# Kernel tuning notes

Hardware: AMD Instinct MI355X
Metric: run time of the kernel (lower is better)

Reference implementation:

```python
import jax, jax.numpy as jnp
import numpy as np

INPUT_DIM = 1024
OUTPUT_DIM = 1000
DEPTH = 10
LAMBDA_REG = 1e-3
N_INTERNAL = 2 ** DEPTH - 1
N_LEAF = 2 ** DEPTH
BATCH = 16384


def setup_inputs() -> dict:
    key = jax.random.key(0)
    k1, k2, k3 = jax.random.split(key, 3)
    X = jax.random.normal(k1, (BATCH, INPUT_DIM), dtype=jnp.float32)
    # torch nn.Linear weight layout: [out_features, in_features]; scaled to keep
    # sigmoid routing probs away from 0/1 saturation (log-reg term).
    W_internal = jax.random.normal(k2, (N_INTERNAL, INPUT_DIM + 1), dtype=jnp.float32) * 0.02
    W_leaf = jax.random.normal(k3, (OUTPUT_DIM, N_LEAF), dtype=jnp.float32) * 0.02
    return {"X": X, "W_internal": W_internal, "W_leaf": W_leaf}


def _tree_paths(X, W_internal):
    B = X.shape[0]
    Xb = jnp.concatenate([jnp.ones((B, 1), X.dtype), X], axis=1)  # [B, D+1]
    logits = jax.nn.sigmoid(Xb @ W_internal.T)                    # [B, N_int]
    routing = jnp.stack([logits, 1.0 - logits], axis=2)           # [B, N_int, 2]
    path = jnp.ones((B, 1), X.dtype)
    reg = jnp.float32(0.0)
    start = 0
    for layer in range(DEPTH):
        n = 2 ** layer
        lp = routing[:, start:start + n, :].reshape(B, 2 * n)     # next_paths [B, 2n]
        path = jnp.repeat(path, 2, axis=1) * lp                   # new path probs [B, 2n]
        # Faithful to source: parent_idx = node_idx // 2 indexes the UPDATED path probs.
        parent = jnp.repeat(path[:, :n], 2, axis=1)               # [B, 2n]
        num = jnp.sum(lp * parent, axis=0)                        # [2n]
        den = jnp.sum(parent, axis=0) + 1e-8                      # [2n]
        alpha = num / den
        factor = LAMBDA_REG * 2.0 ** (-layer)
        reg = reg + factor * jnp.sum(-0.5 * (jnp.log(alpha) + jnp.log(1.0 - alpha)))
        start += n
    return path, reg  # path: [B, 2^DEPTH]


def reference(X, W_internal, W_leaf):
    path_probs, reg = _tree_paths(X, W_internal)
    predictions = path_probs @ W_leaf.T   # [B, output_dim]
    return predictions, reg
```

## Files before the change

kernel.cpp:

```cpp
#include <hip/hip_runtime.h>
#include <hip/hip_bf16.h>

#define B_ROWS 16384
#define K_DIM  1024
#define N_INT  1023
#define N_OUT  1000

using s8vec = __attribute__((ext_vector_type(8))) short;
using f32x4 = __attribute__((ext_vector_type(4))) float;

static const size_t OFF_XB   = 0;
static const size_t OFF_W1   = OFF_XB   + 33554432;
static const size_t OFF_BIAS = OFF_W1   + 2097152;
static const size_t OFF_PROB = OFF_BIAS + 4096;
static const size_t OFF_PATH = OFF_PROB + 33554432;
static const size_t OFF_W2   = OFF_PATH + 33554432;
static const size_t OFF_SG   = OFF_W2   + 2097152;
static const size_t OFF_TKT  = OFF_SG   + 16384;

__device__ __forceinline__ float b2f(ushort u) {
  return __uint_as_float(((unsigned)u) << 16);
}
__device__ __forceinline__ float blo(unsigned u) { return __uint_as_float(u << 16); }
__device__ __forceinline__ float bhi(unsigned u) { return __uint_as_float(u & 0xffff0000u); }
__device__ __forceinline__ ushort f2b(float f) {
  unsigned u = __float_as_uint(f);
  u = u + 0x7FFFu + ((u >> 16) & 1u);
  return (ushort)(u >> 16);
}

__device__ __forceinline__ void load_lds16(const ushort* g, ushort* l) {
  __builtin_amdgcn_global_load_lds((const __attribute__((address_space(1))) void*)g,
                                   (__attribute__((address_space(3))) void*)l,
                                   16, 0, 0);
}

__global__ __launch_bounds__(256) void cvt_all(const float4* __restrict__ X,
                                               ushort4* __restrict__ O,
                                               const float* __restrict__ Wi,
                                               const float* __restrict__ Wl,
                                               ushort* __restrict__ W1,
                                               ushort* __restrict__ W2,
                                               float* __restrict__ bias,
                                               float* __restrict__ Sg,
                                               unsigned* __restrict__ ticket) {
  const int b = blockIdx.x;
  if (b < 16384) {
    const int i = b * 256 + threadIdx.x;
    const float4 v = X[i];
    ushort4 o;
    o.x = f2b(v.x); o.y = f2b(v.y); o.z = f2b(v.z); o.w = f2b(v.w);
    O[i] = o;
  } else if (b < 24576) {
    const int idx = (b - 16384) * 256 + threadIdx.x;
    if (idx < (1 << 20)) {
      const int n = idx >> 10, k = idx & 1023;
      const float v = (n < N_INT) ? Wi[n * 1025 + 1 + k] : 0.f;
      W1[idx] = f2b(v);
      if (k == 0) bias[n] = (n < N_INT) ? Wi[n * 1025] : 0.f;
    } else {
      const int j = idx - (1 << 20);
      const int n = j >> 10, k = j & 1023;
      const float v = (n < N_OUT) ? Wl[n * 1024 + k] : 0.f;
      W2[j] = f2b(v);
    }
  } else {
#pragma unroll
    for (int k = 0; k < 16; ++k) Sg[threadIdx.x + 256 * k] = 0.f;
    if (threadIdx.x == 0) *ticket = 0u;
  }
}

template <int MODE>
__global__ __launch_bounds__(256, 5) void gemm_bt(const ushort* __restrict__ A,
                                                  const ushort* __restrict__ Bm,
                                                  const float* __restrict__ bias,
                                                  void* __restrict__ outp) {
  __shared__ ushort As[2][4096];
  __shared__ ushort Bs[2][4096];
  const int tid = threadIdx.x;
  const int bm = blockIdx.x, bn = blockIdx.y;
  const int lane = tid & 63, wv = tid >> 6;
  const int wm = wv >> 1, wn = wv & 1;
  const int m16 = lane & 15, q = lane >> 4;
  const int qs = q ^ ((m16 >> 1) & 3);

  const int r0 = tid >> 2;
  const int qsw = (tid & 3) ^ ((r0 >> 1) & 3);
  const ushort* aG = A  + (size_t)(bm * 128 + r0) * 1024 + qsw * 8;
  const ushort* bG = Bm + (size_t)(bn * 128 + r0) * 1024 + qsw * 8;

  f32x4 acc[4][4] = {};

#define STAGE(buf, kk) do {                                   \
    load_lds16(aG + (kk), As[buf] + wv * 512);                \
    load_lds16(aG + 65536 + (kk), As[buf] + 2048 + wv * 512); \
    load_lds16(bG + (kk), Bs[buf] + wv * 512);                \
    load_lds16(bG + 65536 + (kk), Bs[buf] + 2048 + wv * 512); \
  } while (0)

#define COMPUTE(cur) do {                                                        \
    s8vec af[4], bfv[4];                                                         \
    _Pragma("unroll")                                                            \
    for (int i = 0; i < 4; ++i)                                                  \
      af[i] = *(const s8vec*)(As[cur] + (wm * 64 + i * 16 + m16) * 32 + qs * 8); \
    _Pragma("unroll")                                                            \
    for (int j = 0; j < 4; ++j)                                                  \
      bfv[j] = *(const s8vec*)(Bs[cur] + (wn * 64 + j * 16 + m16) * 32 + qs * 8);\
    _Pragma("unroll")                                                            \
    for (int i = 0; i < 4; ++i)                                                  \
      _Pragma("unroll")                                                          \
      for (int j = 0; j < 4; ++j)                                                \
        acc[i][j] = __builtin_amdgcn_mfma_f32_16x16x32_bf16(af[i], bfv[j],       \
                                                            acc[i][j], 0, 0, 0);\
  } while (0)

  STAGE(0, 0);
#pragma unroll 1
  for (int k0 = 0; k0 < 992; k0 += 32) {
    const int cur = (k0 >> 5) & 1;
    STAGE(cur ^ 1, k0 + 32);
    asm volatile("s_waitcnt vmcnt(4)\n\ts_barrier" ::: "memory");
    COMPUTE(cur);
    asm volatile("s_barrier" ::: "memory");
  }
  asm volatile("s_waitcnt vmcnt(0)\n\ts_barrier" ::: "memory");
  COMPUTE(1);
#undef STAGE
#undef COMPUTE

  if (MODE == 0) {
    ushort* P = (ushort*)outp;
#pragma unroll
    for (int i = 0; i < 4; ++i)
#pragma unroll
      for (int r = 0; r < 4; ++r) {
        const int gr = bm * 128 + wm * 64 + i * 16 + q * 4 + r;
#pragma unroll
        for (int j = 0; j < 4; ++j) {
          const int gc = bn * 128 + wn * 64 + j * 16 + m16;
          const float z = acc[i][j][r] + bias[gc];
          const float p = __builtin_amdgcn_rcpf(1.f + __expf(-z));
          if (gc < N_INT) P[(size_t)gr * 1024 + gc + 1] = f2b(p);
        }
      }
  } else {
    float* O = (float*)outp;
#pragma unroll
    for (int i = 0; i < 4; ++i)
#pragma unroll
      for (int r = 0; r < 4; ++r) {
        const int gr = bm * 128 + wm * 64 + i * 16 + q * 4 + r;
#pragma unroll
        for (int j = 0; j < 4; ++j) {
          const int gc = bn * 128 + wn * 64 + j * 16 + m16;
          if (gc < N_OUT) O[(size_t)gr * 1000 + gc] = acc[i][j][r];
        }
      }
  }
}

__global__ __launch_bounds__(256) void tree_kernel(const ushort* __restrict__ probs,
                                                   ushort* __restrict__ path,
                                                   float* __restrict__ Spart) {
  __shared__ float Ss[2048];
  for (int i = threadIdx.x; i < 2048; i += 256) Ss[i] = 0.f;
  __syncthreads();
  const int lane = threadIdx.x & 63;
  const int la = lane & 31;
  const int gw = blockIdx.x * 4 + (threadIdx.x >> 6);

  float a19[16] = {}, a29[16] = {};
  float a18[8]  = {}, a28[8]  = {};
  float a17[4]  = {}, a27[4]  = {};
  float a16[2]  = {}, a26[2]  = {};
  float t1[6] = {}, t2[6] = {};

#pragma unroll 1
  for (int rr = 0; rr < 4; ++rr) {
    const int r = gw * 4 + rr;
    const ushort* prow = probs + (size_t)r * 1024;

    const ushort p6 = prow[64 + lane];
    const uint   p7 = *(const uint*)(prow + 128 + 2 * lane);
    const uint2  p8 = *(const uint2*)(prow + 256 + 4 * lane);
    const uint4  p9 = *(const uint4*)(prow + 512 + 8 * lane);
    union { uint4 q[2]; ushort u[16]; } j9;
    j9.q[0] = *(const uint4*)(prow + 512 + 16 * la);
    j9.q[1] = *(const uint4*)(prow + 512 + 16 * la + 8);
    union { uint4 q; ushort u[8]; } j8;
    j8.q = *(const uint4*)(prow + 256 + 8 * la);
    union { uint2 q; ushort u[4]; } j7;
    j7.q = *(const uint2*)(prow + 128 + 4 * la);
    union { uint q; ushort u[2]; } j6;
    j6.q = *(const uint*)(prow + 64 + 2 * la);
    const float q5 = b2f(prow[32 + la]);
    const float q4 = b2f(prow[16 + (lane & 15)]);
    const float q3 = b2f(prow[8 + (lane & 7)]);
    const float q2 = b2f(prow[4 + (lane & 3)]);
    const float q1 = b2f(prow[2 + (lane & 1)]);
    const float q0 = b2f(prow[1]);
    float fac[6];
#pragma unroll
    for (int t = 1; t <= 6; ++t) {
      const int ell = t - 1;
      const int e = lane >> (6 - t);
      const float p = b2f(prow[(1 << ell) + (e >> 1)]);
      fac[ell] = (e & 1) ? (1.f - p) : p;
    }
    const float v = (fac[0] * fac[1]) * (fac[2] * fac[3]) * (fac[4] * fac[5]);

    float w[16];
    { const float p = b2f(p6); w[1] = v * (1.f - p); w[0] = v * p; }
    {
      const float pA = blo(p7), pB = bhi(p7);
      w[3] = w[1] * (1.f - pB); w[2] = w[1] * pB;
      w[1] = w[0] * (1.f - pA); w[0] = w[0] * pA;
    }
    {
      const float pv[4] = { blo(p8.x), bhi(p8.x), blo(p8.y), bhi(p8.y) };
#pragma unroll
      for (int i = 3; i >= 0; --i) {
        w[2 * i + 1] = w[i] * (1.f - pv[i]);
        w[2 * i]     = w[i] * pv[i];
      }
    }
    {
      const uint pv[4] = { p9.x, p9.y, p9.z, p9.w };
#pragma unroll
      for (int i = 7; i >= 0; --i) {
        const float p = (i & 1) ? bhi(pv[i >> 1]) : blo(pv[i >> 1]);
        w[2 * i + 1] = w[i] * (1.f - p);
        w[2 * i]     = w[i] * p;
      }
    }
    union { ushort u[16]; uint4 q4v[2]; } pk;
#pragma unroll
    for (int i = 0; i < 16; ++i) pk.u[i] = f2b(w[i]);
    uint4* dst = (uint4*)(path + (size_t)r * 1024 + lane * 16);
    dst[0] = pk.q4v[0];
    dst[1] = pk.q4v[1];

    float L8[8], L7[4], L6[2];
#pragma unroll
    for (int i = 0; i < 8; ++i) L8[i] = w[2 * i] + w[2 * i + 1];
#pragma unroll
    for (int i = 0; i < 4; ++i) L7[i] = L8[2 * i] + L8[2 * i + 1];
    L6[0] = L7[0] + L7[1]; L6[1] = L7[2] + L7[3];
    const float T = L6[0] + L6[1];

    if (lane < 32) {
#pragma unroll
      for (int i = 0; i < 16; ++i) { a19[i] += w[i];  a29[i] += b2f(j9.u[i]) * w[i]; }
#pragma unroll
      for (int i = 0; i < 8; ++i)  { a18[i] += L8[i]; a28[i] += b2f(j8.u[i]) * L8[i]; }
#pragma unroll
      for (int i = 0; i < 4; ++i)  { a17[i] += L7[i]; a27[i] += b2f(j7.u[i]) * L7[i]; }
#pragma unroll
      for (int i = 0; i < 2; ++i)  { a16[i] += L6[i]; a26[i] += b2f(j6.u[i]) * L6[i]; }
    }

    const float T1 = T  + __shfl_xor(T, 1);
    const float T2 = T1 + __shfl_xor(T1, 2);
    const float T3 = T2 + __shfl_xor(T2, 4);
    const float T4 = T3 + __shfl_xor(T3, 8);
    const float T5 = T4 + __shfl_xor(T4, 16);
    const float v4 = __shfl(T1, (2 * lane) & 63);
    const float v3 = __shfl(T2, (4 * lane) & 63);
    const float v2 = __shfl(T3, (8 * lane) & 63);
    const float v1 = __shfl(T4, (16 * lane) & 63);
    const float v0 = __shfl(T5, 0);
    if (lane < 32) { t1[5] += T;  t2[5] += q5 * T; }
    if (lane < 16) { t1[4] += v4; t2[4] += q4 * v4; }
    if (lane < 8)  { t1[3] += v3; t2[3] += q3 * v3; }
    if (lane < 4)  { t1[2] += v2; t2[2] += q2 * v2; }
    if (lane < 2)  { t1[1] += v1; t2[1] += q1 * v1; }
    if (lane < 1)  { t1[0] += v0; t2[0] += q0 * v0; }
  }

  if (lane < 32) {
#pragma unroll
    for (int i = 0; i < 16; ++i) { atomicAdd(&Ss[511 + 16 * la + i], a19[i]); atomicAdd(&Ss[1535 + 16 * la + i], a29[i]); }
#pragma unroll
    for (int i = 0; i < 8; ++i)  { atomicAdd(&Ss[255 + 8 * la + i],  a18[i]); atomicAdd(&Ss[1279 + 8 * la + i],  a28[i]); }
#pragma unroll
    for (int i = 0; i < 4; ++i)  { atomicAdd(&Ss[127 + 4 * la + i],  a17[i]); atomicAdd(&Ss[1151 + 4 * la + i],  a27[i]); }
#pragma unroll
    for (int i = 0; i < 2; ++i)  { atomicAdd(&Ss[63 + 2 * la + i],   a16[i]); atomicAdd(&Ss[1087 + 2 * la + i],  a26[i]); }
    atomicAdd(&Ss[31 + la], t1[5]); atomicAdd(&Ss[1055 + la], t2[5]);
    if (la < 16) { atomicAdd(&Ss[15 + la], t1[4]); atomicAdd(&Ss[1039 + la], t2[4]); }
    if (la < 8)  { atomicAdd(&Ss[7 + la],  t1[3]); atomicAdd(&Ss[1031 + la], t2[3]); }
    if (la < 4)  { atomicAdd(&Ss[3 + la],  t1[2]); atomicAdd(&Ss[1027 + la], t2[2]); }
    if (la < 2)  { atomicAdd(&Ss[1 + la],  t1[1]); atomicAdd(&Ss[1025 + la], t2[1]); }
    if (la < 1)  { atomicAdd(&Ss[0],       t1[0]); atomicAdd(&Ss[1024],      t2[0]); }
  }
  __syncthreads();
  float* Sp = Spart + (size_t)blockIdx.x * 2048;
  for (int i = threadIdx.x; i < 2048; i += 256) Sp[i] = Ss[i];
}

__global__ __launch_bounds__(256) void reduce_fin(const float* __restrict__ Spart,
                                                  float* __restrict__ Sg,
                                                  float* __restrict__ outreg,
                                                  unsigned* __restrict__ ticket) {
  const int t = threadIdx.x;
  float acc[8] = {};
  const float* base = Spart + (size_t)blockIdx.x * 32 * 2048;
  for (int b = 0; b < 32; ++b) {
    const float* p = base + (size_t)b * 2048;
#pragma unroll
    for (int k = 0; k < 8; ++k) acc[k] += p[t + 256 * k];
  }
#pragma unroll
  for (int k = 0; k < 8; ++k) {
    const int i = t + 256 * k;
    const int node = i & 1023;
    if (node < 1023) atomicAdd(&Sg[(i < 1024 ? 0 : 2048) + node], acc[k]);
  }
  __threadfence();
  __syncthreads();
  __shared__ unsigned rank;
  if (t == 0) rank = atomicAdd(ticket, 1u);
  __syncthreads();
  if (rank == 31) {
    double val = 0.0;
    for (int n = t; n < 1023; n += 256) {
      const int ell = 31 - __clz(n + 1);
      const double s1 = (double)__hip_atomic_load(&Sg[n], __ATOMIC_RELAXED, __HIP_MEMORY_SCOPE_AGENT);
      const double s2 = (double)__hip_atomic_load(&Sg[2048 + n], __ATOMIC_RELAXED, __HIP_MEMORY_SCOPE_AGENT);
      const double den = s1 + 1e-8;
      const double a0 = s2 / den;
      const double a1 = (s1 - s2) / den;
      const double f = 1e-3 * (1.0 / (double)(1 << ell));
      val += -0.5 * f * (log(a0) + log(1.0 - a0) + log(a1) + log(1.0 - a1));
    }
#pragma unroll
    for (int o = 32; o > 0; o >>= 1) val += __shfl_down(val, o, 64);
    __shared__ double partd[4];
    if ((t & 63) == 0) partd[t >> 6] = val;
    __syncthreads();
    if (t == 0) outreg[0] = (float)(partd[0] + partd[1] + partd[2] + partd[3]);
  }
}

extern "C" void kernel_launch(void* const* d_in, const int* in_sizes, int n_in,
                              void* d_out, int out_size, void* d_ws, size_t ws_size,
                              hipStream_t stream) {
  const float* X     = (const float*)d_in[0];
  const float* Wint  = (const float*)d_in[1];
  const float* Wleaf = (const float*)d_in[2];
  float* out = (float*)d_out;
  char* ws = (char*)d_ws;

  ushort* Xb   = (ushort*)(ws + OFF_XB);
  ushort* W1   = (ushort*)(ws + OFF_W1);
  float*  bias = (float*)(ws + OFF_BIAS);
  ushort* prob = (ushort*)(ws + OFF_PROB);
  ushort* path = (ushort*)(ws + OFF_PATH);
  ushort* W2   = (ushort*)(ws + OFF_W2);
  float*  Sg   = (float*)(ws + OFF_SG);
  unsigned* tkt = (unsigned*)(ws + OFF_TKT);
  float*  Spart = (float*)(ws + OFF_XB);

  cvt_all<<<24577, 256, 0, stream>>>((const float4*)X, (ushort4*)Xb,
                                     Wint, Wleaf, W1, W2, bias, Sg, tkt);
  gemm_bt<0><<<dim3(128, 8), 256, 0, stream>>>(Xb, W1, bias, (void*)prob);
  tree_kernel<<<1024, 256, 0, stream>>>(prob, path, Spart);
  gemm_bt<1><<<dim3(128, 8), 256, 0, stream>>>(path, W2, nullptr, (void*)out);
  reduce_fin<<<32, 256, 0, stream>>>(Spart, Sg, out + (size_t)B_ROWS * N_OUT, tkt);
}
```

Baseline: 299.0 us.

## Fuse all stages into one cooperative persistent kernel with grid syncs

Replaces the five separate kernel launches with a single cooperative kernel of 1024 blocks that runs the conversion, first GEMM, tree pass, second GEMM and final reduction in sequence, separated by grid-wide barriers. Shared memory is carved from one 32 KB buffer reused by every stage. The goal is to remove launch gaps and inter-kernel drain/fill overhead. In exchange the conversion stage becomes a strided loop over fewer blocks, the GEMM's occupancy hint drops from 5 to 4, and there is grid.sync overhead. If the cooperative launch fails, the code falls back to the original separate launches.

New measurement: 893.0 us. 2.99x slower.

```diff
diff --git a/kernel.cpp b/kernel.cpp
--- a/kernel.cpp
+++ b/kernel.cpp
@@ -1,5 +1,8 @@
 #include <hip/hip_runtime.h>
 #include <hip/hip_bf16.h>
+#include <hip/hip_cooperative_groups.h>
+
+namespace cg = cooperative_groups;
 
 #define B_ROWS 16384
 #define K_DIM  1024
@@ -35,51 +38,48 @@
                                    16, 0, 0);
 }
 
-__global__ __launch_bounds__(256) void cvt_all(const float4* __restrict__ X,
-                                               ushort4* __restrict__ O,
-                                               const float* __restrict__ Wi,
-                                               const float* __restrict__ Wl,
-                                               ushort* __restrict__ W1,
-                                               ushort* __restrict__ W2,
-                                               float* __restrict__ bias,
-                                               float* __restrict__ Sg,
-                                               unsigned* __restrict__ ticket) {
-  const int b = blockIdx.x;
-  if (b < 16384) {
-    const int i = b * 256 + threadIdx.x;
-    const float4 v = X[i];
-    ushort4 o;
-    o.x = f2b(v.x); o.y = f2b(v.y); o.z = f2b(v.z); o.w = f2b(v.w);
-    O[i] = o;
-  } else if (b < 24576) {
-    const int idx = (b - 16384) * 256 + threadIdx.x;
-    if (idx < (1 << 20)) {
-      const int n = idx >> 10, k = idx & 1023;
-      const float v = (n < N_INT) ? Wi[n * 1025 + 1 + k] : 0.f;
-      W1[idx] = f2b(v);
-      if (k == 0) bias[n] = (n < N_INT) ? Wi[n * 1025] : 0.f;
+
+__device__ __forceinline__ void cvt_stage(int b0, int stride,
+                                          const float4* X, ushort4* O,
+                                          const float* Wi, const float* Wl,
+                                          ushort* W1, ushort* W2, float* bias,
+                                          float* Sg, unsigned* ticket) {
+  for (int b = b0; b < 24577; b += stride) {
+    if (b < 16384) {
+      const int i = b * 256 + threadIdx.x;
+      const float4 v = X[i];
+      ushort4 o;
+      o.x = f2b(v.x); o.y = f2b(v.y); o.z = f2b(v.z); o.w = f2b(v.w);
+      O[i] = o;
+    } else if (b < 24576) {
+      const int idx = (b - 16384) * 256 + threadIdx.x;
+      if (idx < (1 << 20)) {
+        const int n = idx >> 10, k = idx & 1023;
+        const float v = (n < N_INT) ? Wi[n * 1025 + 1 + k] : 0.f;
+        W1[idx] = f2b(v);
+        if (k == 0) bias[n] = (n < N_INT) ? Wi[n * 1025] : 0.f;
+      } else {
+        const int j = idx - (1 << 20);
+        const int n = j >> 10, k = j & 1023;
+        const float v = (n < N_OUT) ? Wl[n * 1024 + k] : 0.f;
+        W2[j] = f2b(v);
+      }
     } else {
-      const int j = idx - (1 << 20);
-      const int n = j >> 10, k = j & 1023;
-      const float v = (n < N_OUT) ? Wl[n * 1024 + k] : 0.f;
-      W2[j] = f2b(v);
-    }
-  } else {
-#pragma unroll
-    for (int k = 0; k < 16; ++k) Sg[threadIdx.x + 256 * k] = 0.f;
-    if (threadIdx.x == 0) *ticket = 0u;
+#pragma unroll
+      for (int k = 0; k < 16; ++k) Sg[threadIdx.x + 256 * k] = 0.f;
+      if (threadIdx.x == 0) *ticket = 0u;
+    }
   }
 }
 
 template <int MODE>
-__global__ __launch_bounds__(256, 5) void gemm_bt(const ushort* __restrict__ A,
-                                                  const ushort* __restrict__ Bm,
-                                                  const float* __restrict__ bias,
-                                                  void* __restrict__ outp) {
-  __shared__ ushort As[2][4096];
-  __shared__ ushort Bs[2][4096];
+__device__ __forceinline__ void gemm_stage(int b, const ushort* A, const ushort* Bm,
+                                           const float* bias, void* outp,
+                                           char* smem) {
+  ushort (*As)[4096] = (ushort (*)[4096])smem;
+  ushort (*Bs)[4096] = (ushort (*)[4096])(smem + 16384);
   const int tid = threadIdx.x;
-  const int bm = blockIdx.x, bn = blockIdx.y;
+  const int bm = b & 127, bn = b >> 7;
   const int lane = tid & 63, wv = tid >> 6;
   const int wm = wv >> 1, wn = wv & 1;
   const int m16 = lane & 15, q = lane >> 4;
@@ -160,15 +160,14 @@
   }
 }
 
-__global__ __launch_bounds__(256) void tree_kernel(const ushort* __restrict__ probs,
-                                                   ushort* __restrict__ path,
-                                                   float* __restrict__ Spart) {
-  __shared__ float Ss[2048];
+__device__ __forceinline__ void tree_stage(int blk, const ushort* probs,
+                                           ushort* path, float* Spart, char* smem) {
+  float* Ss = (float*)smem;
   for (int i = threadIdx.x; i < 2048; i += 256) Ss[i] = 0.f;
   __syncthreads();
   const int lane = threadIdx.x & 63;
   const int la = lane & 31;
-  const int gw = blockIdx.x * 4 + (threadIdx.x >> 6);
+  const int gw = blk * 4 + (threadIdx.x >> 6);
 
   float a19[16] = {}, a29[16] = {};
   float a18[8]  = {}, a28[8]  = {};
@@ -295,17 +294,15 @@
     if (la < 1)  { atomicAdd(&Ss[0],       t1[0]); atomicAdd(&Ss[1024],      t2[0]); }
   }
   __syncthreads();
-  float* Sp = Spart + (size_t)blockIdx.x * 2048;
+  float* Sp = Spart + (size_t)blk * 2048;
   for (int i = threadIdx.x; i < 2048; i += 256) Sp[i] = Ss[i];
 }
 
-__global__ __launch_bounds__(256) void reduce_fin(const float* __restrict__ Spart,
-                                                  float* __restrict__ Sg,
-                                                  float* __restrict__ outreg,
-                                                  unsigned* __restrict__ ticket) {
+__device__ __forceinline__ void reduce_stage(int blk, const float* Spart, float* Sg,
+                                             float* outreg, unsigned* ticket, char* smem) {
   const int t = threadIdx.x;
   float acc[8] = {};
-  const float* base = Spart + (size_t)blockIdx.x * 32 * 2048;
+  const float* base = Spart + (size_t)blk * 32 * 2048;
   for (int b = 0; b < 32; ++b) {
     const float* p = base + (size_t)b * 2048;
 #pragma unroll
@@ -319,10 +316,11 @@
   }
   __threadfence();
   __syncthreads();
-  __shared__ unsigned rank;
-  if (t == 0) rank = atomicAdd(ticket, 1u);
+  unsigned* rank = (unsigned*)smem;
+  double* partd = (double*)(smem + 64);
+  if (t == 0) *rank = atomicAdd(ticket, 1u);
   __syncthreads();
-  if (rank == 31) {
+  if (*rank == 31) {
     double val = 0.0;
     for (int n = t; n < 1023; n += 256) {
       const int ell = 31 - __clz(n + 1);
@@ -336,22 +334,18 @@
     }
 #pragma unroll
     for (int o = 32; o > 0; o >>= 1) val += __shfl_down(val, o, 64);
-    __shared__ double partd[4];
     if ((t & 63) == 0) partd[t >> 6] = val;
     __syncthreads();
     if (t == 0) outreg[0] = (float)(partd[0] + partd[1] + partd[2] + partd[3]);
   }
 }
 
-extern "C" void kernel_launch(void* const* d_in, const int* in_sizes, int n_in,
-                              void* d_out, int out_size, void* d_ws, size_t ws_size,
-                              hipStream_t stream) {
-  const float* X     = (const float*)d_in[0];
-  const float* Wint  = (const float*)d_in[1];
-  const float* Wleaf = (const float*)d_in[2];
-  float* out = (float*)d_out;
-  char* ws = (char*)d_ws;
-
+__global__ __launch_bounds__(256, 4) void fused_all(const float* Xf,
+                                                    const float* Wi,
+                                                    const float* Wl,
+                                                    char* ws,
+                                                    float* out) {
+  __shared__ __align__(16) char smem[32768];
   ushort* Xb   = (ushort*)(ws + OFF_XB);
   ushort* W1   = (ushort*)(ws + OFF_W1);
   float*  bias = (float*)(ws + OFF_BIAS);
@@ -361,11 +355,69 @@
   float*  Sg   = (float*)(ws + OFF_SG);
   unsigned* tkt = (unsigned*)(ws + OFF_TKT);
   float*  Spart = (float*)(ws + OFF_XB);
-
-  cvt_all<<<24577, 256, 0, stream>>>((const float4*)X, (ushort4*)Xb,
-                                     Wint, Wleaf, W1, W2, bias, Sg, tkt);
-  gemm_bt<0><<<dim3(128, 8), 256, 0, stream>>>(Xb, W1, bias, (void*)prob);
-  tree_kernel<<<1024, 256, 0, stream>>>(prob, path, Spart);
-  gemm_bt<1><<<dim3(128, 8), 256, 0, stream>>>(path, W2, nullptr, (void*)out);
-  reduce_fin<<<32, 256, 0, stream>>>(Spart, Sg, out + (size_t)B_ROWS * N_OUT, tkt);
-}
+  const int b = blockIdx.x;
+  cg::grid_group grid = cg::this_grid();
+
+  cvt_stage(b, 1024, (const float4*)Xf, (ushort4*)Xb, Wi, Wl, W1, W2, bias, Sg, tkt);
+  grid.sync();
+  gemm_stage<0>(b, Xb, W1, bias, (void*)prob, smem);
+  grid.sync();
+  tree_stage(b, prob, path, Spart, smem);
+  grid.sync();
+  gemm_stage<1>(b, path, W2, nullptr, (void*)out, smem);
+  grid.sync();
+  if (b < 32) reduce_stage(b, Spart, Sg, out + (size_t)B_ROWS * N_OUT, tkt, smem);
+}
+
+__global__ __launch_bounds__(256) void cvt_all_k(const float4* X, ushort4* O,
+                                                 const float* Wi, const float* Wl,
+                                                 ushort* W1, ushort* W2, float* bias,
+                                                 float* Sg, unsigned* ticket) {
+  cvt_stage(blockIdx.x, 1 << 30, X, O, Wi, Wl, W1, W2, bias, Sg, ticket);
+}
+template <int MODE>
+__global__ __launch_bounds__(256, 4) void gemm_k(const ushort* A, const ushort* Bm,
+                                                 const float* bias, void* outp) {
+  __shared__ __align__(16) char smem[32768];
+  gemm_stage<MODE>(blockIdx.x + 128 * blockIdx.y, A, Bm, bias, outp, smem);
+}
+__global__ __launch_bounds__(256) void tree_k(const ushort* probs, ushort* path, float* Spart) {
+  __shared__ __align__(16) char smem[8192];
+  tree_stage(blockIdx.x, probs, path, Spart, smem);
+}
+__global__ __launch_bounds__(256) void reduce_k(const float* Spart, float* Sg,
+                                                float* outreg, unsigned* ticket) {
+  __shared__ __align__(16) char smem[128];
+  reduce_stage(blockIdx.x, Spart, Sg, outreg, ticket, smem);
+}
+
+extern "C" void kernel_launch(void* const* d_in, const int* in_sizes, int n_in,
+                              void* d_out, int out_size, void* d_ws, size_t ws_size,
+                              hipStream_t stream) {
+  const float* X     = (const float*)d_in[0];
+  const float* Wint  = (const float*)d_in[1];
+  const float* Wleaf = (const float*)d_in[2];
+  float* out = (float*)d_out;
+  char* ws = (char*)d_ws;
+
+  void* kargs[] = { (void*)&X, (void*)&Wint, (void*)&Wleaf, (void*)&ws, (void*)&out };
+  hipError_t e = hipLaunchCooperativeKernel((const void*)fused_all,
+                                            dim3(1024), dim3(256), kargs, 0, stream);
+  if (e != hipSuccess) {
+    ushort* Xb   = (ushort*)(ws + OFF_XB);
+    ushort* W1   = (ushort*)(ws + OFF_W1);
+    float*  bias = (float*)(ws + OFF_BIAS);
+    ushort* prob = (ushort*)(ws + OFF_PROB);
+    ushort* path = (ushort*)(ws + OFF_PATH);
+    ushort* W2   = (ushort*)(ws + OFF_W2);
+    float*  Sg   = (float*)(ws + OFF_SG);
+    unsigned* tkt = (unsigned*)(ws + OFF_TKT);
+    float*  Spart = (float*)(ws + OFF_XB);
+    cvt_all_k<<<24577, 256, 0, stream>>>((const float4*)X, (ushort4*)Xb,
+                                         Wint, Wleaf, W1, W2, bias, Sg, tkt);
+    gemm_k<0><<<dim3(128, 8), 256, 0, stream>>>(Xb, W1, bias, (void*)prob);
+    tree_k<<<1024, 256, 0, stream>>>(prob, path, Spart);
+    gemm_k<1><<<dim3(128, 8), 256, 0, stream>>>(path, W2, nullptr, (void*)out);
+    reduce_k<<<32, 256, 0, stream>>>(Spart, Sg, out + (size_t)B_ROWS * N_OUT, tkt);
+  }
+}
```
